# Optimization experiments

Measured on AMD Instinct MI355X. Metric: run time of the kernel, lower is better.

The kernel has to match this reference:

```python
import jax, jax.numpy as jnp
import numpy as np

N_QUBITS = 13
DEPTH = 4
DIM = 2 ** N_QUBITS
PI = 3.141592653589793

# qubit 0 = most significant bit of the basis-state index
_idx = np.arange(DIM)
BITS = np.stack([(_idx >> (N_QUBITS - 1 - q)) & 1 for q in range(N_QUBITS)], axis=1)  # (DIM, n)
SIGNS = jnp.asarray(1.0 - 2.0 * BITS, dtype=jnp.float32)                               # Z eigenvalues, (DIM, n)
PARITY = jnp.asarray((-1.0) ** BITS.sum(axis=1), dtype=jnp.float32)                    # <Z^{(x)n}> diagonal, (DIM,)
# CZ entangling chain (q, q+1): diagonal (-1)^{sum_q b_q b_{q+1}}
ENT = jnp.asarray((-1.0) ** (BITS[:, :-1] * BITS[:, 1:]).sum(axis=1), dtype=jnp.float32)


def fwht(psi):
    """Normalized fast Walsh-Hadamard transform (H on every qubit), psi: (B, DIM) complex."""
    B = psi.shape[0]
    for q in range(N_QUBITS):
        psi = psi.reshape(B, 2 ** q, 2, -1)
        psi = jnp.stack([psi[:, :, 0] + psi[:, :, 1], psi[:, :, 0] - psi[:, :, 1]], axis=2)
    return psi.reshape(B, DIM) * (2.0 ** (-N_QUBITS / 2))


def feature_map_state(x):
    """Havlicek ZZ feature map: psi = D(x) H^n D(x) H^n |0...0>.
    Diagonal phase per basis state b: sum_j x_j s_j(b) + sum_{j<k} (pi-x_j)(pi-x_k) s_j(b) s_k(b)."""
    a = PI - x                                              # (B, n)
    u = x @ SIGNS.T                                         # (B, DIM)
    v = a @ SIGNS.T                                         # (B, DIM)
    phi = u + 0.5 * (v * v - jnp.sum(a * a, axis=1, keepdims=True))  # pair term via (sum)^2 trick
    d = jnp.exp(1j * phi)                                   # complex64 diagonal
    psi = jnp.full((x.shape[0], DIM), DIM ** -0.5, dtype=jnp.complex64)  # H^n |0>
    psi = fwht(d * psi)
    return d * psi


def _apply_1q(psi, U, q):
    """Apply 2x2 complex gate U to qubit q (bit-sliced)."""
    B = psi.shape[0]
    psi = psi.reshape(B, 2 ** q, 2, -1)
    a0, a1 = psi[:, :, 0], psi[:, :, 1]
    out = jnp.stack([U[0, 0] * a0 + U[0, 1] * a1, U[1, 0] * a0 + U[1, 1] * a1], axis=2)
    return out.reshape(B, DIM)


def variational_apply(psi, theta):
    """(DEPTH+1) layers of per-qubit Rz(b)Ry(a), CZ-chain entanglers between layers."""
    th = theta.reshape(DEPTH + 1, N_QUBITS, 2)
    for l in range(DEPTH + 1):
        if l > 0:
            psi = psi * ENT
        for q in range(N_QUBITS):
            ca = jnp.cos(0.5 * th[l, q, 0])
            sa = jnp.sin(0.5 * th[l, q, 0])
            em = jnp.exp(-0.5j * th[l, q, 1])
            ep = jnp.exp(0.5j * th[l, q, 1])
            U = jnp.stack([jnp.stack([em * ca, -em * sa]), jnp.stack([ep * sa, ep * ca])])
            psi = _apply_1q(psi, U, q)
    return psi


def setup_inputs() -> dict:
    key = jax.random.key(0)
    k1, k2 = jax.random.split(key)
    x = jax.random.normal(k1, (512, N_QUBITS), dtype=jnp.float32)
    theta = 0.1 * jax.random.normal(k2, ((DEPTH + 1) * N_QUBITS * 2,), dtype=jnp.float32)
    bias = jnp.zeros((1,), dtype=jnp.float32)
    return {"x": x, "theta": theta, "bias": bias}


def reference(x, theta, bias):
    psi = feature_map_state(x)
    psi = variational_apply(psi, theta)
    prob = psi.real ** 2 + psi.imag ** 2              # (B, DIM)
    logit = prob @ PARITY + bias[0]                   # (B,)
    return jnp.stack([-logit, logit], axis=1)         # two-class logits
```

## Files before the change

kernel.cpp:

```cpp
#include <hip/hip_runtime.h>
#include <hip/hip_fp16.h>

#define NQ   13
#define DIM  8192
#define PI_F 3.14159265358979323846f
#define NT   512
#define NAMP 16

#define NSLOT 9712

__device__ __forceinline__ int base0(int t) { return 16 * t + 4 * (t >> 1) + 16 * (t >> 4); }
__device__ __forceinline__ int slot1f(int t, int j) {
  return 304 * (t >> 4) + (t & 15) + 16 * j + 4 * (j >> 1);
}
__device__ __forceinline__ int slot2f(int t, int j) {
  return 4864 * (t >> 8) + (t & 255) + 4 * ((t >> 5) & 7) + 304 * j;
}
__device__ __forceinline__ int base3(int t) { return 8 * t + 4 * (t >> 2) + 16 * (t >> 5); }

union F4H { float4 f; __half2 h[4]; };

__device__ __forceinline__ void rsincos(float x, float* s, float* c) {
  const float INV2PI = 0.15915494309189535f;
  const float TWOPI  = 6.283185307179586f;
  float r = x * INV2PI;
  r -= rintf(r);
  float ang = r * TWOPI;
  *s = __sinf(ang);
  *c = __cosf(ang);
}

__device__ __forceinline__ void waveFence() {
  __builtin_amdgcn_wave_barrier();
  __threadfence_block();
  __builtin_amdgcn_wave_barrier();
}

__device__ __forceinline__ float2 f2fma(float s, float2 a, float2 b) {
  return make_float2(fmaf(s, a.x, b.x), fmaf(s, a.y, b.y));
}
__device__ __forceinline__ float2 f2add(float2 a, float2 b) {
  return make_float2(a.x + b.x, a.y + b.y);
}
__device__ __forceinline__ float2 f2sub(float2 a, float2 b) {
  return make_float2(a.x - b.x, a.y - b.y);
}
__device__ __forceinline__ float2 cphase(float2 v, float cs, float sn) {
  return make_float2(fmaf(cs, v.x, -sn * v.y), fmaf(cs, v.y, sn * v.x));
}
__device__ __forceinline__ float2 cmul(float2 a, float2 b) {
  return make_float2(fmaf(a.x, b.x, -a.y * b.y), fmaf(a.x, b.y, a.y * b.x));
}

__device__ __forceinline__ void loadA0f(const __half2* __restrict__ sAmp, int t, float2* amp) {
  const __half2* p = sAmp + base0(t);
  #pragma unroll
  for (int k = 0; k < 4; k++) {
    F4H u; u.f = *reinterpret_cast<const float4*>(p + 4 * k);
    #pragma unroll
    for (int c = 0; c < 4; c++) amp[4 * k + c] = __half22float2(u.h[c]);
  }
}
__device__ __forceinline__ void storeA0f(__half2* __restrict__ sAmp, int t, const float2* amp) {
  __half2* p = sAmp + base0(t);
  #pragma unroll
  for (int k = 0; k < 4; k++) {
    F4H u;
    #pragma unroll
    for (int c = 0; c < 4; c++) u.h[c] = __float22half2_rn(amp[4 * k + c]);
    *reinterpret_cast<float4*>(p + 4 * k) = u.f;
  }
}

__device__ __forceinline__ void loadA3f(const __half2* __restrict__ sAmp, int t, float2* amp) {
  const __half2* p = sAmp + base3(t);
  #pragma unroll
  for (int k = 0; k < 2; k++) {
    F4H u; u.f = *reinterpret_cast<const float4*>(p + 4 * k);
    #pragma unroll
    for (int c = 0; c < 4; c++) amp[4 * k + c] = __half22float2(u.h[c]);
  }
  p += 4864;
  #pragma unroll
  for (int k = 0; k < 2; k++) {
    F4H u; u.f = *reinterpret_cast<const float4*>(p + 4 * k);
    #pragma unroll
    for (int c = 0; c < 4; c++) amp[8 + 4 * k + c] = __half22float2(u.h[c]);
  }
}
__device__ __forceinline__ void storeA3f(__half2* __restrict__ sAmp, int t, const float2* amp) {
  __half2* p = sAmp + base3(t);
  #pragma unroll
  for (int k = 0; k < 2; k++) {
    F4H u;
    #pragma unroll
    for (int c = 0; c < 4; c++) u.h[c] = __float22half2_rn(amp[4 * k + c]);
    *reinterpret_cast<float4*>(p + 4 * k) = u.f;
  }
  p += 4864;
  #pragma unroll
  for (int k = 0; k < 2; k++) {
    F4H u;
    #pragma unroll
    for (int c = 0; c < 4; c++) u.h[c] = __float22half2_rn(amp[8 + 4 * k + c]);
    *reinterpret_cast<float4*>(p + 4 * k) = u.f;
  }
}

__device__ __forceinline__ void loadA1h(const __half2* __restrict__ sAmp, int t, __half2* amp) {
  #pragma unroll
  for (int j = 0; j < NAMP; j++) amp[j] = sAmp[slot1f(t, j)];
}
__device__ __forceinline__ void storeA1h(__half2* __restrict__ sAmp, int t, const __half2* amp) {
  #pragma unroll
  for (int j = 0; j < NAMP; j++) sAmp[slot1f(t, j)] = amp[j];
}
__device__ __forceinline__ void loadA2h(const __half2* __restrict__ sAmp, int t, __half2* amp) {
  #pragma unroll
  for (int j = 0; j < NAMP; j++) amp[j] = sAmp[slot2f(t, j)];
}
__device__ __forceinline__ void storeA2h(__half2* __restrict__ sAmp, int t, const __half2* amp) {
  #pragma unroll
  for (int j = 0; j < NAMP; j++) sAmp[slot2f(t, j)] = amp[j];
}
__device__ __forceinline__ void loadA2f(const __half2* __restrict__ sAmp, int t, float2* amp) {
  #pragma unroll
  for (int j = 0; j < NAMP; j++) amp[j] = __half22float2(sAmp[slot2f(t, j)]);
}
__device__ __forceinline__ void storeA2f(__half2* __restrict__ sAmp, int t, const float2* amp) {
  #pragma unroll
  for (int j = 0; j < NAMP; j++) sAmp[slot2f(t, j)] = __float22half2_rn(amp[j]);
}

template<int KB>
__device__ __forceinline__ void fwht_bit(float2* amp) {
  #pragma unroll
  for (int j = 0; j < NAMP; j++) if (!(j & (1 << KB))) {
    int j1 = j | (1 << KB);
    float2 a0 = amp[j], a1 = amp[j1];
    amp[j]  = f2add(a0, a1);
    amp[j1] = f2sub(a0, a1);
  }
}
template<int KB>
__device__ __forceinline__ void applyRy(float2* amp, float ta, float sa) {
  #pragma unroll
  for (int j = 0; j < NAMP; j++) if (!(j & (1 << KB))) {
    int j1 = j | (1 << KB);
    amp[j]  = f2fma(-ta, amp[j1], amp[j]);
    amp[j1] = f2fma( sa, amp[j],  amp[j1]);
    amp[j]  = f2fma(-ta, amp[j1], amp[j]);
  }
}

template<int KB>
__device__ __forceinline__ void fwht_bitH(__half2* amp) {
  #pragma unroll
  for (int j = 0; j < NAMP; j++) if (!(j & (1 << KB))) {
    int j1 = j | (1 << KB);
    __half2 a0 = amp[j], a1 = amp[j1];
    amp[j]  = __hadd2(a0, a1);
    amp[j1] = __hsub2(a0, a1);
  }
}
template<int KB>
__device__ __forceinline__ void applyRyH(__half2* amp, __half2 nta, __half2 sa) {
  #pragma unroll
  for (int j = 0; j < NAMP; j++) if (!(j & (1 << KB))) {
    int j1 = j | (1 << KB);
    amp[j]  = __hfma2(nta, amp[j1], amp[j]);
    amp[j1] = __hfma2(sa,  amp[j],  amp[j1]);
    amp[j]  = __hfma2(nta, amp[j1], amp[j]);
  }
}

template<int PAT>
__device__ __forceinline__ void buildTree(const float* __restrict__ w, float bias,
                                          int t, float* s) {
  float base = bias;
  constexpr int B0 = (PAT == 0) ? 4 : 3;
  #pragma unroll
  for (int k = 0; k < 9; k++) base += ((t >> k) & 1) ? w[B0 + k] : 0.0f;
  constexpr int P[4] = { 0, 1, 2, (PAT == 0) ? 3 : 12 };
  s[0] = base;
  #pragma unroll
  for (int k = 0; k < 4; k++) {
    float wp = w[P[k]];
    #pragma unroll
    for (int m = 0; m < (1 << k); m++) s[m | (1 << k)] = s[m] + wp;
  }
}

template<int PAT, bool INIT>
__device__ __forceinline__ void featureDiag(float2* amp,
                                            const float* __restrict__ wX,
                                            const float* __restrict__ wA,
                                            const float* __restrict__ cons, int t) {
  float u[NAMP], v[NAMP];
  buildTree<PAT>(wX, cons[0], t, u);
  buildTree<PAT>(wA, cons[1], t, v);
  float A2 = cons[2];
  #pragma unroll
  for (int j = 0; j < NAMP; j++) {
    float phi = u[j] + 0.5f * (v[j] * v[j] - A2);
    float sn, cs; rsincos(phi, &sn, &cs);
    if constexpr (INIT) amp[j] = make_float2(cs, sn);
    else                amp[j] = cphase(amp[j], cs, sn);
  }
}

__device__ __forceinline__ void applyDiagW0(float2* amp,
                                            const float* __restrict__ wb,
                                            const float* __restrict__ eR,
                                            const float* __restrict__ eI,
                                            float bias, int t) {
  float base = bias;
  #pragma unroll
  for (int k = 0; k < 9; k++) base += ((t >> k) & 1) ? wb[4 + k] : 0.0f;
  float2 c[16];
  { float sn, cs; rsincos(base, &sn, &cs); c[0] = make_float2(cs, sn); }
  #pragma unroll
  for (int k = 0; k < 4; k++) {
    float2 e = make_float2(eR[k], eI[k]);
    #pragma unroll
    for (int m = 0; m < (1 << k); m++) c[m | (1 << k)] = cmul(c[m], e);
  }
  #pragma unroll
  for (int j = 0; j < 16; j++) {
    int i = (t << 4) | j;
    float sgn = (__popc(i & (i >> 1)) & 1) ? -1.0f : 1.0f;
    amp[j] = cphase(amp[j], c[j].x * sgn, c[j].y * sgn);
  }
}

__global__ __launch_bounds__(NT, 4) void qc_kernel(
    const float* __restrict__ xin,
    const float* __restrict__ thin,
    const float* __restrict__ bin,
    float* __restrict__ out) {
  __shared__ alignas(16) __half2 sAmp[NSLOT];
  __shared__ float gTA[65], gSA[65];
  __shared__ __half2 hNTA[65], hSA[65];
  __shared__ float gBbit[65];
  __shared__ float eBr[65], eBi[65];
  __shared__ float wX[13], wA[13];
  __shared__ float cons[8];
  __shared__ float red[NT / 64];

  const int t = threadIdx.x;
  const int b = blockIdx.x;

  if (t < NQ) {
    float xq = xin[b * NQ + t];
    float aq = PI_F - xq;
    wX[12 - t] = -2.0f * xq;
    wA[12 - t] = -2.0f * aq;
  }
  if (t < 65) {
    float av = thin[2 * t];
    float bv = thin[2 * t + 1];
    float ca = cosf(0.5f * av);
    float sa = sinf(0.5f * av);
    float ta = sa / (1.0f + ca);
    gTA[t] = ta;
    gSA[t] = sa;
    hNTA[t] = __float2half2_rn(-ta);
    hSA[t]  = __float2half2_rn(sa);
    int l = t / NQ, q = t % NQ;
    int s = l * NQ + (12 - q);
    gBbit[s] = bv;
    eBr[s] = cosf(bv);
    eBi[s] = sinf(bv);
  }
  __syncthreads();
  if (t == 0) {
    float X = 0.f, A = 0.f, A2 = 0.f;
    for (int p = 0; p < NQ; p++) {
      float xq = -0.5f * wX[p], aq = -0.5f * wA[p];
      X += xq; A += aq; A2 += aq * aq;
    }
    cons[0] = X; cons[1] = A; cons[2] = A2;
    for (int l = 0; l < 5; l++) {
      float s = 0.f;
      for (int p = 0; p < NQ; p++) s += gBbit[l * NQ + p];
      cons[3 + l] = -0.5f * s;
    }
  }
  __syncthreads();

  {
    float2 amp[NAMP];
    featureDiag<0, true>(amp, wX, wA, cons, t);
    fwht_bit<0>(amp); fwht_bit<1>(amp); fwht_bit<2>(amp); fwht_bit<3>(amp);
    storeA0f(sAmp, t, amp);
  }
  waveFence();

  {
    __half2 amp[NAMP];
    loadA1h(sAmp, t, amp);
    fwht_bitH<0>(amp); fwht_bitH<1>(amp); fwht_bitH<2>(amp); fwht_bitH<3>(amp);
    storeA1h(sAmp, t, amp);
  }
  __syncthreads();

  {
    float2 amp[NAMP];
    loadA2f(sAmp, t, amp);
    fwht_bit<0>(amp); fwht_bit<1>(amp); fwht_bit<2>(amp); fwht_bit<3>(amp);
    storeA2f(sAmp, t, amp);
  }
  __syncthreads();

  {
    float2 amp[NAMP];
    loadA3f(sAmp, t, amp);
    fwht_bit<3>(amp);
    featureDiag<3, false>(amp, wX, wA, cons, t);
    applyRy<0>(amp, gTA[12], gSA[12]);
    applyRy<1>(amp, gTA[11], gSA[11]);
    applyRy<2>(amp, gTA[10], gSA[10]);
    applyRy<3>(amp, gTA[0],  gSA[0]);
    storeA3f(sAmp, t, amp);
  }
  __syncthreads();

  float acc = 0.0f;
  for (int l = 0; l < 5; l++) {
    const int g = l * NQ;
    if (l > 0) {
      float2 amp[NAMP];
      loadA3f(sAmp, t, amp);
      applyRy<0>(amp, gTA[g + 12], gSA[g + 12]);
      applyRy<1>(amp, gTA[g + 11], gSA[g + 11]);
      applyRy<2>(amp, gTA[g + 10], gSA[g + 10]);
      applyRy<3>(amp, gTA[g + 0],  gSA[g + 0]);
      storeA3f(sAmp, t, amp);
      __syncthreads();
    }
    {
      __half2 amp[NAMP];
      loadA2h(sAmp, t, amp);
      applyRyH<0>(amp, hNTA[g + 4], hSA[g + 4]);
      applyRyH<1>(amp, hNTA[g + 3], hSA[g + 3]);
      applyRyH<2>(amp, hNTA[g + 2], hSA[g + 2]);
      applyRyH<3>(amp, hNTA[g + 1], hSA[g + 1]);
      storeA2h(sAmp, t, amp);
    }
    __syncthreads();
    {
      __half2 amp[NAMP];
      loadA1h(sAmp, t, amp);
      applyRyH<0>(amp, hNTA[g + 8], hSA[g + 8]);
      applyRyH<1>(amp, hNTA[g + 7], hSA[g + 7]);
      applyRyH<2>(amp, hNTA[g + 6], hSA[g + 6]);
      applyRyH<3>(amp, hNTA[g + 5], hSA[g + 5]);
      storeA1h(sAmp, t, amp);
    }
    waveFence();
    {
      float2 amp[NAMP];
      loadA0f(sAmp, t, amp);
      applyRy<3>(amp, gTA[g + 9], gSA[g + 9]);
      if (l < 4) {
        applyDiagW0(amp, gBbit + g, eBr + g, eBi + g, cons[3 + l], t);
        storeA0f(sAmp, t, amp);
      } else {
        int pt = __popc(t) & 1;
        #pragma unroll
        for (int j = 0; j < NAMP; j++) {
          float p2 = fmaf(amp[j].x, amp[j].x, amp[j].y * amp[j].y);
          acc += ((pt + __popc(j)) & 1) ? -p2 : p2;
        }
      }
    }
    if (l < 4) __syncthreads();
  }

  #pragma unroll
  for (int off = 32; off > 0; off >>= 1) acc += __shfl_down(acc, off, 64);
  if ((t & 63) == 0) red[t >> 6] = acc;
  __syncthreads();
  if (t == 0) {
    float total = 0.f;
    #pragma unroll
    for (int w = 0; w < NT / 64; w++) total += red[w];
    float logit = total * (1.0f / 67108864.0f) + bin[0];
    out[b * 2 + 0] = -logit;
    out[b * 2 + 1] = logit;
  }
}

extern "C" void kernel_launch(void* const* d_in, const int* in_sizes, int n_in,
                              void* d_out, int out_size, void* d_ws, size_t ws_size,
                              hipStream_t stream) {
  const float* x  = (const float*)d_in[0];
  const float* th = (const float*)d_in[1];
  const float* bi = (const float*)d_in[2];
  float* out = (float*)d_out;
  int B = in_sizes[0] / NQ;
  qc_kernel<<<B, NT, 0, stream>>>(x, th, bi, out);
}
```

Baseline: 90.47 us.

## Replace shared-memory qubit passes with cross-lane DPP/shuffle butterflies and two-layout scheme

Restructures the state-vector passes so that qubits mapped to lane bits are processed in registers via DPP and shfl_xor butterflies, in both the Walsh-Hadamard transform and the Ry gates. This cuts the shared-memory round trips from four layouts to two, with vectorised float4 accesses, and removes one barrier per layer. The Ry gates on lane bits use a cos/sin form with lane-dependent signs, and the feature diagonal and entangler indexing are remapped to the new layout. The trade-off is many more cross-lane permute instructions and some half-precision arithmetic where float was used before, which may affect accuracy.

```diff
diff --git a/kernel.cpp b/kernel.cpp
--- a/kernel.cpp
+++ b/kernel.cpp
@@ -7,16 +7,13 @@
 #define NT   512
 #define NAMP 16
 
-#define NSLOT 9712
-
-__device__ __forceinline__ int base0(int t) { return 16 * t + 4 * (t >> 1) + 16 * (t >> 4); }
-__device__ __forceinline__ int slot1f(int t, int j) {
-  return 304 * (t >> 4) + (t & 15) + 16 * j + 4 * (j >> 1);
-}
-__device__ __forceinline__ int slot2f(int t, int j) {
-  return 4864 * (t >> 8) + (t & 255) + 4 * ((t >> 5) & 7) + 304 * j;
-}
-__device__ __forceinline__ int base3(int t) { return 8 * t + 4 * (t >> 2) + 16 * (t >> 5); }
+#define NSLOT 9216
+
+__device__ __forceinline__ int baseA(int t) { return 16 * t + 4 * (t >> 1); }
+__device__ __forceinline__ int baseB(int t, int g) {
+  int m = t & 31;
+  return 4 * m + 4 * (m >> 3) + 144 * ((t >> 6) & 7) + 1152 * ((t >> 5) & 1) + 2304 * g;
+}
 
 union F4H { float4 f; __half2 h[4]; };
 
@@ -30,12 +27,6 @@
   *c = __cosf(ang);
 }
 
-__device__ __forceinline__ void waveFence() {
-  __builtin_amdgcn_wave_barrier();
-  __threadfence_block();
-  __builtin_amdgcn_wave_barrier();
-}
-
 __device__ __forceinline__ float2 f2fma(float s, float2 a, float2 b) {
   return make_float2(fmaf(s, a.x, b.x), fmaf(s, a.y, b.y));
 }
@@ -52,84 +43,63 @@
   return make_float2(fmaf(a.x, b.x, -a.y * b.y), fmaf(a.x, b.y, a.y * b.x));
 }
 
-__device__ __forceinline__ void loadA0f(const __half2* __restrict__ sAmp, int t, float2* amp) {
-  const __half2* p = sAmp + base0(t);
+template<int MASK>
+__device__ __forceinline__ int xorLaneI(int x) {
+  if constexpr (MASK == 1)
+    return __builtin_amdgcn_update_dpp(x, x, 0xB1, 0xF, 0xF, false);
+  else if constexpr (MASK == 2)
+    return __builtin_amdgcn_update_dpp(x, x, 0x4E, 0xF, 0xF, false);
+  else
+    return __shfl_xor(x, MASK, 64);
+}
+template<int MASK>
+__device__ __forceinline__ __half2 xorLaneH(__half2 v) {
+  union { __half2 h; int i; } u; u.h = v;
+  u.i = xorLaneI<MASK>(u.i);
+  return u.h;
+}
+template<int MASK>
+__device__ __forceinline__ float xorLaneF(float v) {
+  union { float f; int i; } u; u.f = v;
+  u.i = xorLaneI<MASK>(u.i);
+  return u.f;
+}
+
+__device__ __forceinline__ void loadAh(const __half2* __restrict__ sAmp, int t, __half2* amp) {
+  const __half2* p = sAmp + baseA(t);
   #pragma unroll
   for (int k = 0; k < 4; k++) {
     F4H u; u.f = *reinterpret_cast<const float4*>(p + 4 * k);
     #pragma unroll
-    for (int c = 0; c < 4; c++) amp[4 * k + c] = __half22float2(u.h[c]);
-  }
-}
-__device__ __forceinline__ void storeA0f(__half2* __restrict__ sAmp, int t, const float2* amp) {
-  __half2* p = sAmp + base0(t);
+    for (int c = 0; c < 4; c++) amp[4 * k + c] = u.h[c];
+  }
+}
+__device__ __forceinline__ void storeAh(__half2* __restrict__ sAmp, int t, const __half2* amp) {
+  __half2* p = sAmp + baseA(t);
   #pragma unroll
   for (int k = 0; k < 4; k++) {
     F4H u;
     #pragma unroll
-    for (int c = 0; c < 4; c++) u.h[c] = __float22half2_rn(amp[4 * k + c]);
+    for (int c = 0; c < 4; c++) u.h[c] = amp[4 * k + c];
     *reinterpret_cast<float4*>(p + 4 * k) = u.f;
   }
 }
-
-__device__ __forceinline__ void loadA3f(const __half2* __restrict__ sAmp, int t, float2* amp) {
-  const __half2* p = sAmp + base3(t);
-  #pragma unroll
-  for (int k = 0; k < 2; k++) {
-    F4H u; u.f = *reinterpret_cast<const float4*>(p + 4 * k);
-    #pragma unroll
-    for (int c = 0; c < 4; c++) amp[4 * k + c] = __half22float2(u.h[c]);
-  }
-  p += 4864;
-  #pragma unroll
-  for (int k = 0; k < 2; k++) {
-    F4H u; u.f = *reinterpret_cast<const float4*>(p + 4 * k);
-    #pragma unroll
-    for (int c = 0; c < 4; c++) amp[8 + 4 * k + c] = __half22float2(u.h[c]);
-  }
-}
-__device__ __forceinline__ void storeA3f(__half2* __restrict__ sAmp, int t, const float2* amp) {
-  __half2* p = sAmp + base3(t);
-  #pragma unroll
-  for (int k = 0; k < 2; k++) {
+__device__ __forceinline__ void loadBh(const __half2* __restrict__ sAmp, int t, __half2* amp) {
+  #pragma unroll
+  for (int g = 0; g < 4; g++) {
+    F4H u; u.f = *reinterpret_cast<const float4*>(sAmp + baseB(t, g));
+    #pragma unroll
+    for (int c = 0; c < 4; c++) amp[4 * g + c] = u.h[c];
+  }
+}
+__device__ __forceinline__ void storeBh(__half2* __restrict__ sAmp, int t, const __half2* amp) {
+  #pragma unroll
+  for (int g = 0; g < 4; g++) {
     F4H u;
     #pragma unroll
-    for (int c = 0; c < 4; c++) u.h[c] = __float22half2_rn(amp[4 * k + c]);
-    *reinterpret_cast<float4*>(p + 4 * k) = u.f;
-  }
-  p += 4864;
-  #pragma unroll
-  for (int k = 0; k < 2; k++) {
-    F4H u;
-    #pragma unroll
-    for (int c = 0; c < 4; c++) u.h[c] = __float22half2_rn(amp[8 + 4 * k + c]);
-    *reinterpret_cast<float4*>(p + 4 * k) = u.f;
-  }
-}
-
-__device__ __forceinline__ void loadA1h(const __half2* __restrict__ sAmp, int t, __half2* amp) {
-  #pragma unroll
-  for (int j = 0; j < NAMP; j++) amp[j] = sAmp[slot1f(t, j)];
-}
-__device__ __forceinline__ void storeA1h(__half2* __restrict__ sAmp, int t, const __half2* amp) {
-  #pragma unroll
-  for (int j = 0; j < NAMP; j++) sAmp[slot1f(t, j)] = amp[j];
-}
-__device__ __forceinline__ void loadA2h(const __half2* __restrict__ sAmp, int t, __half2* amp) {
-  #pragma unroll
-  for (int j = 0; j < NAMP; j++) amp[j] = sAmp[slot2f(t, j)];
-}
-__device__ __forceinline__ void storeA2h(__half2* __restrict__ sAmp, int t, const __half2* amp) {
-  #pragma unroll
-  for (int j = 0; j < NAMP; j++) sAmp[slot2f(t, j)] = amp[j];
-}
-__device__ __forceinline__ void loadA2f(const __half2* __restrict__ sAmp, int t, float2* amp) {
-  #pragma unroll
-  for (int j = 0; j < NAMP; j++) amp[j] = __half22float2(sAmp[slot2f(t, j)]);
-}
-__device__ __forceinline__ void storeA2f(__half2* __restrict__ sAmp, int t, const float2* amp) {
-  #pragma unroll
-  for (int j = 0; j < NAMP; j++) sAmp[slot2f(t, j)] = __float22half2_rn(amp[j]);
+    for (int c = 0; c < 4; c++) u.h[c] = amp[4 * g + c];
+    *reinterpret_cast<float4*>(sAmp + baseB(t, g)) = u.f;
+  }
 }
 
 template<int KB>
@@ -153,24 +123,30 @@
   }
 }
 
-template<int KB>
-__device__ __forceinline__ void fwht_bitH(__half2* amp) {
-  #pragma unroll
-  for (int j = 0; j < NAMP; j++) if (!(j & (1 << KB))) {
-    int j1 = j | (1 << KB);
-    __half2 a0 = amp[j], a1 = amp[j1];
-    amp[j]  = __hadd2(a0, a1);
-    amp[j1] = __hsub2(a0, a1);
-  }
-}
-template<int KB>
-__device__ __forceinline__ void applyRyH(__half2* amp, __half2 nta, __half2 sa) {
-  #pragma unroll
-  for (int j = 0; j < NAMP; j++) if (!(j & (1 << KB))) {
-    int j1 = j | (1 << KB);
-    amp[j]  = __hfma2(nta, amp[j1], amp[j]);
-    amp[j1] = __hfma2(sa,  amp[j],  amp[j1]);
-    amp[j]  = __hfma2(nta, amp[j1], amp[j]);
+template<int MASK>
+__device__ __forceinline__ void laneRyH(__half2* amp, __half2 c2, __half2 spm) {
+  #pragma unroll
+  for (int j = 0; j < NAMP; j++) {
+    __half2 p = xorLaneH<MASK>(amp[j]);
+    amp[j] = __hfma2(spm, p, __hmul2(c2, amp[j]));
+  }
+}
+template<int MASK>
+__device__ __forceinline__ void laneFwhtH(__half2* amp, __half2 sgn) {
+  #pragma unroll
+  for (int j = 0; j < NAMP; j++) {
+    __half2 p = xorLaneH<MASK>(amp[j]);
+    amp[j] = __hfma2(sgn, amp[j], p);
+  }
+}
+template<int MASK>
+__device__ __forceinline__ void laneFwhtF(float2* amp, float sgn) {
+  #pragma unroll
+  for (int j = 0; j < NAMP; j++) {
+    float px = xorLaneF<MASK>(amp[j].x);
+    float py = xorLaneF<MASK>(amp[j].y);
+    amp[j].x = fmaf(sgn, amp[j].x, px);
+    amp[j].y = fmaf(sgn, amp[j].y, py);
   }
 }
 
@@ -178,14 +154,20 @@
 __device__ __forceinline__ void buildTree(const float* __restrict__ w, float bias,
                                           int t, float* s) {
   float base = bias;
-  constexpr int B0 = (PAT == 0) ? 4 : 3;
-  #pragma unroll
-  for (int k = 0; k < 9; k++) base += ((t >> k) & 1) ? w[B0 + k] : 0.0f;
-  constexpr int P[4] = { 0, 1, 2, (PAT == 0) ? 3 : 12 };
+  if constexpr (PAT == 0) {
+    #pragma unroll
+    for (int k = 0; k < 9; k++) base += ((t >> k) & 1) ? w[4 + k] : 0.0f;
+  } else {
+    constexpr int BM[9] = {2, 3, 4, 5, 6, 10, 7, 8, 9};
+    #pragma unroll
+    for (int k = 0; k < 9; k++) base += ((t >> k) & 1) ? w[BM[k]] : 0.0f;
+  }
+  constexpr int PA[4] = {0, 1, 2, 3};
+  constexpr int PB[4] = {0, 1, 11, 12};
   s[0] = base;
   #pragma unroll
   for (int k = 0; k < 4; k++) {
-    float wp = w[P[k]];
+    float wp = w[(PAT == 0) ? PA[k] : PB[k]];
     #pragma unroll
     for (int m = 0; m < (1 << k); m++) s[m | (1 << k)] = s[m] + wp;
   }
@@ -209,11 +191,11 @@
   }
 }
 
-__device__ __forceinline__ void applyDiagW0(float2* amp,
-                                            const float* __restrict__ wb,
-                                            const float* __restrict__ eR,
-                                            const float* __restrict__ eI,
-                                            float bias, int t) {
+__device__ __forceinline__ void applyDiagA(float2* amp,
+                                           const float* __restrict__ wb,
+                                           const float* __restrict__ eR,
+                                           const float* __restrict__ eI,
+                                           float bias, int t) {
   float base = bias;
   #pragma unroll
   for (int k = 0; k < 9; k++) base += ((t >> k) & 1) ? wb[4 + k] : 0.0f;
@@ -225,10 +207,12 @@
     #pragma unroll
     for (int m = 0; m < (1 << k); m++) c[m | (1 << k)] = cmul(c[m], e);
   }
+  int st = __popc(t & (t >> 1)) & 1;
+  int tb = t & 1;
   #pragma unroll
   for (int j = 0; j < 16; j++) {
-    int i = (t << 4) | j;
-    float sgn = (__popc(i & (i >> 1)) & 1) ? -1.0f : 1.0f;
+    int sgb = st ^ (((j >> 3) & tb)) ^ (__popc(j & (j >> 1)) & 1);
+    float sgn = sgb ? -1.0f : 1.0f;
     amp[j] = cphase(amp[j], c[j].x * sgn, c[j].y * sgn);
   }
 }
@@ -240,7 +224,7 @@
     float* __restrict__ out) {
   __shared__ alignas(16) __half2 sAmp[NSLOT];
   __shared__ float gTA[65], gSA[65];
-  __shared__ __half2 hNTA[65], hSA[65];
+  __shared__ __half2 hC2[65], hS2[65];
   __shared__ float gBbit[65];
   __shared__ float eBr[65], eBi[65];
   __shared__ float wX[13], wA[13];
@@ -248,6 +232,7 @@
   __shared__ float red[NT / 64];
 
   const int t = threadIdx.x;
+  const int lane = t & 63;
   const int b = blockIdx.x;
 
   if (t < NQ) {
@@ -264,8 +249,8 @@
     float ta = sa / (1.0f + ca);
     gTA[t] = ta;
     gSA[t] = sa;
-    hNTA[t] = __float2half2_rn(-ta);
-    hSA[t]  = __float2half2_rn(sa);
+    hC2[t] = __float2half2_rn(ca);
+    hS2[t] = __float2half2_rn(sa);
     int l = t / NQ, q = t % NQ;
     int s = l * NQ + (12 - q);
     gBbit[s] = bv;
@@ -292,79 +277,67 @@
     float2 amp[NAMP];
     featureDiag<0, true>(amp, wX, wA, cons, t);
     fwht_bit<0>(amp); fwht_bit<1>(amp); fwht_bit<2>(amp); fwht_bit<3>(amp);
-    storeA0f(sAmp, t, amp);
-  }
-  waveFence();
+    laneFwhtF<1>(amp, (lane & 1) ? -1.0f : 1.0f);
+    __half2 h[NAMP];
+    #pragma unroll
+    for (int j = 0; j < NAMP; j++) h[j] = __float22half2_rn(amp[j]);
+    const __half2 P1 = __float2half2_rn(1.0f), M1 = __float2half2_rn(-1.0f);
+    laneFwhtH<2>(h,  (lane & 2)  ? M1 : P1);
+    laneFwhtH<4>(h,  (lane & 4)  ? M1 : P1);
+    laneFwhtH<8>(h,  (lane & 8)  ? M1 : P1);
+    laneFwhtH<16>(h, (lane & 16) ? M1 : P1);
+    laneFwhtH<32>(h, (lane & 32) ? M1 : P1);
+    storeAh(sAmp, t, h);
+  }
+  __syncthreads();
 
   {
-    __half2 amp[NAMP];
-    loadA1h(sAmp, t, amp);
-    fwht_bitH<0>(amp); fwht_bitH<1>(amp); fwht_bitH<2>(amp); fwht_bitH<3>(amp);
-    storeA1h(sAmp, t, amp);
-  }
-  __syncthreads();
-
-  {
+    __half2 h[NAMP];
+    loadBh(sAmp, t, h);
     float2 amp[NAMP];
-    loadA2f(sAmp, t, amp);
-    fwht_bit<0>(amp); fwht_bit<1>(amp); fwht_bit<2>(amp); fwht_bit<3>(amp);
-    storeA2f(sAmp, t, amp);
-  }
-  __syncthreads();
-
-  {
-    float2 amp[NAMP];
-    loadA3f(sAmp, t, amp);
-    fwht_bit<3>(amp);
-    featureDiag<3, false>(amp, wX, wA, cons, t);
-    applyRy<0>(amp, gTA[12], gSA[12]);
-    applyRy<1>(amp, gTA[11], gSA[11]);
-    applyRy<2>(amp, gTA[10], gSA[10]);
-    applyRy<3>(amp, gTA[0],  gSA[0]);
-    storeA3f(sAmp, t, amp);
+    #pragma unroll
+    for (int j = 0; j < NAMP; j++) amp[j] = __half22float2(h[j]);
+    laneFwhtF<32>(amp, (lane & 32) ? -1.0f : 1.0f);
+    fwht_bit<2>(amp); fwht_bit<3>(amp);
+    featureDiag<1, false>(amp, wX, wA, cons, t);
+    applyRy<2>(amp, gTA[1], gSA[1]);
+    applyRy<3>(amp, gTA[0], gSA[0]);
+    #pragma unroll
+    for (int j = 0; j < NAMP; j++) h[j] = __float22half2_rn(amp[j]);
+    __half2 s2 = hS2[2];
+    __half2 spm = (lane & 32) ? s2 : __hneg2(s2);
+    laneRyH<32>(h, hC2[2], spm);
+    storeBh(sAmp, t, h);
   }
   __syncthreads();
 
   float acc = 0.0f;
   for (int l = 0; l < 5; l++) {
     const int g = l * NQ;
-    if (l > 0) {
+    {
+      __half2 h[NAMP];
+      loadAh(sAmp, t, h);
+      {
+        __half2 s2, spm;
+        s2 = hS2[g + 8]; spm = (lane & 1)  ? s2 : __hneg2(s2); laneRyH<1>(h,  hC2[g + 8], spm);
+        s2 = hS2[g + 7]; spm = (lane & 2)  ? s2 : __hneg2(s2); laneRyH<2>(h,  hC2[g + 7], spm);
+        s2 = hS2[g + 6]; spm = (lane & 4)  ? s2 : __hneg2(s2); laneRyH<4>(h,  hC2[g + 6], spm);
+        s2 = hS2[g + 5]; spm = (lane & 8)  ? s2 : __hneg2(s2); laneRyH<8>(h,  hC2[g + 5], spm);
+        s2 = hS2[g + 4]; spm = (lane & 16) ? s2 : __hneg2(s2); laneRyH<16>(h, hC2[g + 4], spm);
+        s2 = hS2[g + 3]; spm = (lane & 32) ? s2 : __hneg2(s2); laneRyH<32>(h, hC2[g + 3], spm);
+      }
       float2 amp[NAMP];
-      loadA3f(sAmp, t, amp);
+      #pragma unroll
+      for (int j = 0; j < NAMP; j++) amp[j] = __half22float2(h[j]);
       applyRy<0>(amp, gTA[g + 12], gSA[g + 12]);
       applyRy<1>(amp, gTA[g + 11], gSA[g + 11]);
       applyRy<2>(amp, gTA[g + 10], gSA[g + 10]);
-      applyRy<3>(amp, gTA[g + 0],  gSA[g + 0]);
-      storeA3f(sAmp, t, amp);
-      __syncthreads();
-    }
-    {
-      __half2 amp[NAMP];
-      loadA2h(sAmp, t, amp);
-      applyRyH<0>(amp, hNTA[g + 4], hSA[g + 4]);
-      applyRyH<1>(amp, hNTA[g + 3], hSA[g + 3]);
-      applyRyH<2>(amp, hNTA[g + 2], hSA[g + 2]);
-      applyRyH<3>(amp, hNTA[g + 1], hSA[g + 1]);
-      storeA2h(sAmp, t, amp);
-    }
-    __syncthreads();
-    {
-      __half2 amp[NAMP];
-      loadA1h(sAmp, t, amp);
-      applyRyH<0>(amp, hNTA[g + 8], hSA[g + 8]);
-      applyRyH<1>(amp, hNTA[g + 7], hSA[g + 7]);
-      applyRyH<2>(amp, hNTA[g + 6], hSA[g + 6]);
-      applyRyH<3>(amp, hNTA[g + 5], hSA[g + 5]);
-      storeA1h(sAmp, t, amp);
-    }
-    waveFence();
-    {
-      float2 amp[NAMP];
-      loadA0f(sAmp, t, amp);
-      applyRy<3>(amp, gTA[g + 9], gSA[g + 9]);
+      applyRy<3>(amp, gTA[g + 9],  gSA[g + 9]);
       if (l < 4) {
-        applyDiagW0(amp, gBbit + g, eBr + g, eBi + g, cons[3 + l], t);
-        storeA0f(sAmp, t, amp);
+        applyDiagA(amp, gBbit + g, eBr + g, eBi + g, cons[3 + l], t);
+        #pragma unroll
+        for (int j = 0; j < NAMP; j++) h[j] = __float22half2_rn(amp[j]);
+        storeAh(sAmp, t, h);
       } else {
         int pt = __popc(t) & 1;
         #pragma unroll
@@ -374,7 +347,26 @@
         }
       }
     }
-    if (l < 4) __syncthreads();
+    if (l < 4) {
+      __syncthreads();
+      const int g1 = g + NQ;
+      {
+        __half2 h[NAMP];
+        loadBh(sAmp, t, h);
+        __half2 s2 = hS2[g1 + 2];
+        __half2 spm = (lane & 32) ? s2 : __hneg2(s2);
+        laneRyH<32>(h, hC2[g1 + 2], spm);
+        float2 amp[NAMP];
+        #pragma unroll
+        for (int j = 0; j < NAMP; j++) amp[j] = __half22float2(h[j]);
+        applyRy<2>(amp, gTA[g1 + 1], gSA[g1 + 1]);
+        applyRy<3>(amp, gTA[g1 + 0], gSA[g1 + 0]);
+        #pragma unroll
+        for (int j = 0; j < NAMP; j++) h[j] = __float22half2_rn(amp[j]);
+        storeBh(sAmp, t, h);
+      }
+      __syncthreads();
+    }
   }
 
   #pragma unroll
```

Measured after the change: 102.5 us. 1.13x slower.
